# Kernel tuning notes

Measured on AMD Instinct MI355X. Metric: run time of the kernel, lower is better.

The kernel has to match this reference:

```python
import jax, jax.numpy as jnp
import numpy as np

# DeBut factor chain: each entry is [output_size, input_size, row, col, diag]
R_SHAPES = [[2048, 2048, 4, 4, 1],
            [2048, 2048, 8, 8, 4],
            [1024, 2048, 4, 8, 32],
            [512, 1024, 8, 16, 64]]
K = 4          # kernel_size
PAD = 0        # padding
IN_SIZE = 512 * K  # input_channel * kernel_size = 2048
NUM_PARAMS = sum(o * c for (o, _, _, c, _) in R_SHAPES)  # 40960


def setup_inputs() -> dict:
    key = jax.random.key(0)
    k1, k2, k3 = jax.random.split(key, 3)
    x = jax.random.normal(k1, (16, 512, 2048), dtype=jnp.float32)
    twiddle = jax.random.normal(k2, (NUM_PARAMS,), dtype=jnp.float32) * (1.0 / np.sqrt(2.0))
    bound = 1.0 / np.sqrt(IN_SIZE)
    bias = jax.random.uniform(k3, (512,), dtype=jnp.float32, minval=-bound, maxval=bound)
    return {"x": x, "twiddle": twiddle, "bias": bias}


def _pre_process(x):
    # x: (B, C, L) -> im2col rows (B*l_out, K*C), matching torch unfold + permute(0,3,2,1)
    B, C, L = x.shape
    l_out = L + 2 * PAD - (K - 1)
    xp = jnp.pad(x, ((0, 0), (0, 0), (PAD, PAD)))
    # (B, C, K, l_out): window offset axis (small fixed loop over K)
    win = jnp.stack([xp[:, :, i:i + l_out] for i in range(K)], axis=2)
    # -> (B, l_out, K, C) -> (B*l_out, K*C)
    return win.transpose(0, 3, 2, 1).reshape(B * l_out, K * C), l_out


def _debut_mult(rows, twiddle):
    # rows: (N, in_size); chain of block-diagonal butterfly factors
    out = rows
    p = 0
    for (osz, isz, row, col, diag) in R_SHAPES:
        g = isz // (col * diag)          # number of blocks
        n_p = col * osz
        # t: (g, row, col, diag)
        t = twiddle[p:p + n_p].reshape(g, diag, row, col).transpose(0, 2, 3, 1)
        xr = out.reshape(-1, g, col, diag)
        # contract over col within each block: (N, g, row, diag)
        out = jnp.einsum('grcd,bgcd->bgrd', t, xr)
        p += n_p
    return out.reshape(out.shape[0], -1)  # (N, out_size)


def reference(x, twiddle, bias):
    B, C, L = x.shape
    rows, l_out = _pre_process(x)
    out = _debut_mult(rows, twiddle) + bias
    # (B, l_out, out_channel) -> (B, out_channel, l_out)
    return out.reshape(B, l_out, -1).transpose(0, 2, 1)
```

## Files before the change

kernel.cpp:

```cpp
#include <hip/hip_runtime.h>

#define L_IN   2048
#define C_IN   512
#define L_OUT  2045
#define XT_PAD 21
#define CS     520
#define DS2    1218
#define AS2    38

typedef short short8 __attribute__((ext_vector_type(8)));
typedef float float4v __attribute__((ext_vector_type(4)));

__device__ __forceinline__ unsigned short bf16r(float f) {
    unsigned u = __float_as_uint(f);
    unsigned r = (u + 0x7FFFu + ((u >> 16) & 1u)) >> 16;
    return (unsigned short)r;
}

__global__ __launch_bounds__(256)
void build_wf(const float* __restrict__ tw, unsigned short* __restrict__ W21f,
              unsigned short* __restrict__ W43f) {
    int id = blockIdx.x * 256 + threadIdx.x;
    if (id < 65536) {
        int p = id & 7, lane = (id >> 3) & 63, oh = (id >> 9) & 1, g = id >> 10;
        int a = oh * 16 + (lane & 15);
        int e = ((lane >> 4) & 3) * 8 + p;
        int r2 = a >> 2, d2 = a & 3, c2 = e >> 2, c1 = e & 3;
        float v = tw[8192 + ((g * 4 + d2) * 8 + r2) * 8 + c2]
                * tw[(g * 8 + c2) * 16 + d2 * 4 + c1];
        W21f[id] = bf16r(v);
    } else if (id < 98304) {
        int id2 = id - 65536;
        int p = id2 & 7, lane = (id2 >> 3) & 63, kh = (id2 >> 9) & 1, s = id2 >> 10;
        int u = lane & 15;
        int w = kh * 32 + ((lane >> 4) & 3) * 8 + p;
        int r4 = u >> 1, hi = u & 1, d4 = hi * 32 + s, p2 = w >> 3, c3 = w & 7;
        float v = 0.f;
        #pragma unroll
        for (int lo = 0; lo < 2; ++lo)
            v += tw[32768 + (d4 * 8 + r4) * 16 + (2 * p2 + lo)]
               * tw[24576 + ((p2 * 32 + s) * 4 + (2 * lo + hi)) * 8 + c3];
        W43f[id2] = bf16r(v);
    }
}

__global__ __launch_bounds__(512)
void debut_fused_mfma(const unsigned short* __restrict__ W21f,
                      const unsigned short* __restrict__ W43f,
                      const float* __restrict__ x,
                      const float* __restrict__ bias, float* __restrict__ out) {
    __shared__ unsigned short xtile[20 * CS];
    __shared__ unsigned int   out2[9736];

    const int bid = blockIdx.x;
    const int swz = (bid & 7) * 256 + (bid >> 3);
    const int lt = swz & 127, b = swz >> 7;
    const int l0 = lt * 16;
    const int t = threadIdx.x;
    const int lane = t & 63, wv = t >> 6;
    const int lr = lane & 15, lh = lane >> 4;

    const float* xb = x + (size_t)b * C_IN * L_IN;

    {
        const int lq = t & 3;
        #pragma unroll
        for (int pass = 0; pass < 4; ++pass) {
            int cc = pass * 128 + (t >> 2);
            float4 v = *reinterpret_cast<const float4*>(xb + (size_t)cc * L_IN + l0 + lq * 4);
            int base = (lq * 4) * CS + cc;
            xtile[base         ] = bf16r(v.x);
            xtile[base + CS    ] = bf16r(v.y);
            xtile[base + 2 * CS] = bf16r(v.z);
            xtile[base + 3 * CS] = bf16r(v.w);
        }
        int cc = t;
        int lx = l0 + 16; if (lx > L_IN - 4) lx = L_IN - 4;
        float4 v = *reinterpret_cast<const float4*>(xb + (size_t)cc * L_IN + lx);
        int base = 16 * CS + cc;
        xtile[base         ] = bf16r(v.x);
        xtile[base + CS    ] = bf16r(v.y);
        xtile[base + 2 * CS] = bf16r(v.z);
        xtile[base + 3 * CS] = bf16r(v.w);
    }

    short8 wa[4][2];
    #pragma unroll
    for (int si = 0; si < 4; ++si) {
        int s = wv * 4 + si;
        wa[si][0] = *(const short8*)(W43f + ((size_t)(s * 2 + 0) * 64 + lane) * 8);
        wa[si][1] = *(const short8*)(W43f + ((size_t)(s * 2 + 1) * 64 + lane) * 8);
    }

    __syncthreads();

    float4v accB[4] = {};

    #pragma unroll
    for (int p = 0; p < 2; ++p) {
        const int koff = 2 * p + (wv >> 2);
        const unsigned short* xrow = &xtile[(lr + koff) * CS + lh * 8];

        #pragma unroll
        for (int gi = 0; gi < 4; ++gi) {
            const int gp = wv * 4 + gi;
            const int g  = p * 32 + gp;
            short8 vfrag = *(const short8*)(xrow + (gp & 15) * 32);
            #pragma unroll
            for (int oh = 0; oh < 2; ++oh) {
                short8 wfrag = *(const short8*)(W21f + ((size_t)(g * 2 + oh) * 64 + lane) * 8);
                float4v acc = {};
                acc = __builtin_amdgcn_mfma_f32_16x16x32_bf16(vfrag, wfrag, acc, 0, 0, 0);
                const int a = oh * 16 + lr;
                unsigned d0 = (unsigned)bf16r(acc[0]) | ((unsigned)bf16r(acc[1]) << 16);
                unsigned d1 = (unsigned)bf16r(acc[2]) | ((unsigned)bf16r(acc[3]) << 16);
                out2[(lh * 2 + 0) * DS2 + a * AS2 + gp] = d0;
                out2[(lh * 2 + 1) * DS2 + a * AS2 + gp] = d1;
            }
        }
        __syncthreads();

        #pragma unroll
        for (int si = 0; si < 4; ++si) {
            const int s = wv * 4 + si;
            const int rb = (lr >> 1) * DS2 + s * AS2 + lh * 8;
            uint2 q0 = *(const uint2*)&out2[rb + 0];
            uint2 q1 = *(const uint2*)&out2[rb + 2];
            uint2 q2 = *(const uint2*)&out2[rb + 4];
            uint2 q3 = *(const uint2*)&out2[rb + 6];
            unsigned w0, w1, w2, w3;
            if (lr & 1) {
                w0 = (q0.x >> 16) | (q0.y & 0xffff0000u);
                w1 = (q1.x >> 16) | (q1.y & 0xffff0000u);
                w2 = (q2.x >> 16) | (q2.y & 0xffff0000u);
                w3 = (q3.x >> 16) | (q3.y & 0xffff0000u);
            } else {
                w0 = (q0.x & 0xffffu) | (q0.y << 16);
                w1 = (q1.x & 0xffffu) | (q1.y << 16);
                w2 = (q2.x & 0xffffu) | (q2.y << 16);
                w3 = (q3.x & 0xffffu) | (q3.y << 16);
            }
            uint4 uw{w0, w1, w2, w3};
            short8 bb = *reinterpret_cast<short8*>(&uw);
            accB[si] = __builtin_amdgcn_mfma_f32_16x16x32_bf16(wa[si][p], bb, accB[si], 0, 0, 0);
        }
        if (p == 0) __syncthreads();
    }

    const int lpos = l0 + lr;
    if (lpos < L_OUT) {
        #pragma unroll
        for (int si = 0; si < 4; ++si) {
            const int s = wv * 4 + si;
            #pragma unroll
            for (int i = 0; i < 4; ++i) {
                int o4 = s + 32 * (lh * 4 + i);
                out[((size_t)(b * 512 + o4)) * L_OUT + lpos] = accB[si][i] + bias[o4];
            }
        }
    }
}

__global__ __launch_bounds__(256)
void debut_fused_kernel(const float* __restrict__ x,
                        const float* __restrict__ tw,
                        const float* __restrict__ bias,
                        float* __restrict__ out)
{
    __shared__ float xt[C_IN * XT_PAD];
    __shared__ float bufA[2048];
    __shared__ float bufB[2048];
    const int tile = blockIdx.x, b = blockIdx.y;
    const int l0 = tile * 16;
    const int tid = threadIdx.x;
    const float* xb = x + (size_t)b * C_IN * L_IN;
    for (int idx = tid; idx < C_IN * 19; idx += 256) {
        int c = idx / 19, ll = idx - c * 19, l = l0 + ll;
        xt[c * XT_PAD + ll] = (l < L_IN) ? xb[c * L_IN + l] : 0.0f;
    }
    __syncthreads();
    const float* t1 = tw; const float* t2 = tw + 8192;
    const float* t3 = tw + 24576; const float* t4 = tw + 32768;
    for (int rr = 0; rr < 16; ++rr) {
        const int l = l0 + rr;
        if (l >= L_OUT) break;
        #pragma unroll
        for (int i = 0; i < 8; ++i) {
            int o = tid + 256 * i, gb = o >> 2, k = gb >> 7, cb = (gb & 127) << 2;
            const float4 tq = *reinterpret_cast<const float4*>(t1 + o * 4);
            const float* xp = &xt[cb * XT_PAD + rr + k];
            bufA[o] = tq.x * xp[0] + tq.y * xp[XT_PAD] + tq.z * xp[2 * XT_PAD] + tq.w * xp[3 * XT_PAD];
        }
        __syncthreads();
        #pragma unroll
        for (int i = 0; i < 8; ++i) {
            int o = tid + 256 * i, gb = o >> 5, r = (o >> 2) & 7, d = o & 3;
            const float* tp = t2 + (((gb << 2) + d) * 8 + r) * 8;
            const float* ip = &bufA[(gb << 5) + d];
            float acc = 0.0f;
            #pragma unroll
            for (int c = 0; c < 8; ++c) acc += tp[c] * ip[c << 2];
            bufB[o] = acc;
        }
        __syncthreads();
        #pragma unroll
        for (int i = 0; i < 4; ++i) {
            int o = tid + 256 * i, gb = o >> 7, r = (o >> 5) & 3, d = o & 31;
            const float* tp = t3 + (((gb << 5) + d) * 4 + r) * 8;
            const float* ip = &bufB[(gb << 8) + d];
            float acc = 0.0f;
            #pragma unroll
            for (int c = 0; c < 8; ++c) acc += tp[c] * ip[c << 5];
            bufA[o] = acc;
        }
        __syncthreads();
        #pragma unroll
        for (int i = 0; i < 2; ++i) {
            int o = tid + 256 * i, r = o >> 6, d = o & 63;
            const float* tp = t4 + ((d << 3) + r) * 16;
            float acc = 0.0f;
            #pragma unroll
            for (int c = 0; c < 16; ++c) acc += tp[c] * bufA[(c << 6) + d];
            out[((size_t)(b * 512 + o)) * L_OUT + l] = acc + bias[o];
        }
        __syncthreads();
    }
}

extern "C" void kernel_launch(void* const* d_in, const int* in_sizes, int n_in,
                              void* d_out, int out_size, void* d_ws, size_t ws_size,
                              hipStream_t stream) {
    const float* x    = (const float*)d_in[0];
    const float* tw   = (const float*)d_in[1];
    const float* bias = (const float*)d_in[2];
    float* out = (float*)d_out;

    const size_t W21_B = 65536 * 2;
    const size_t W43_B = 32768 * 2;

    if (ws_size < W21_B + W43_B) {
        dim3 grid(128, 16);
        debut_fused_kernel<<<grid, dim3(256), 0, stream>>>(x, tw, bias, out);
        return;
    }

    unsigned short* W21f = (unsigned short*)d_ws;
    unsigned short* W43f = (unsigned short*)((char*)d_ws + W21_B);

    build_wf<<<dim3(384), dim3(256), 0, stream>>>(tw, W21f, W43f);
    debut_fused_mfma<<<dim3(2048), dim3(512), 0, stream>>>(W21f, W43f, x, bias, out);
}
```

Baseline: 46.26 us.

## Process two L-tiles per block and prefetch the next x tile during compute

Each block now handles two consecutive 16-wide L tiles, halving the grid to 1024 blocks. It loads the second tile's x data into registers while computing the first tile, then writes it to shared memory after storing the first tile's output. The aim is to hide global load latency and amortise the W43 fragment loads and block setup over two tiles. The cost is higher register pressure from the prefetch buffer and fewer blocks for occupancy and tail balance.

```diff
diff --git a/kernel.cpp b/kernel.cpp
--- a/kernel.cpp
+++ b/kernel.cpp
@@ -45,44 +45,22 @@
 }
 
 __global__ __launch_bounds__(512)
-void debut_fused_mfma(const unsigned short* __restrict__ W21f,
-                      const unsigned short* __restrict__ W43f,
-                      const float* __restrict__ x,
-                      const float* __restrict__ bias, float* __restrict__ out) {
+void debut_fused2(const unsigned short* __restrict__ W21f,
+                  const unsigned short* __restrict__ W43f,
+                  const float* __restrict__ x,
+                  const float* __restrict__ bias, float* __restrict__ out) {
     __shared__ unsigned short xtile[20 * CS];
     __shared__ unsigned int   out2[9736];
 
     const int bid = blockIdx.x;
-    const int swz = (bid & 7) * 256 + (bid >> 3);
-    const int lt = swz & 127, b = swz >> 7;
-    const int l0 = lt * 16;
+    const int swz = (bid & 7) * 128 + (bid >> 3);
+    const int ltp = swz & 63, b = swz >> 6;
     const int t = threadIdx.x;
     const int lane = t & 63, wv = t >> 6;
     const int lr = lane & 15, lh = lane >> 4;
+    const int lq = t & 3, ccq = t >> 2;
 
     const float* xb = x + (size_t)b * C_IN * L_IN;
-
-    {
-        const int lq = t & 3;
-        #pragma unroll
-        for (int pass = 0; pass < 4; ++pass) {
-            int cc = pass * 128 + (t >> 2);
-            float4 v = *reinterpret_cast<const float4*>(xb + (size_t)cc * L_IN + l0 + lq * 4);
-            int base = (lq * 4) * CS + cc;
-            xtile[base         ] = bf16r(v.x);
-            xtile[base + CS    ] = bf16r(v.y);
-            xtile[base + 2 * CS] = bf16r(v.z);
-            xtile[base + 3 * CS] = bf16r(v.w);
-        }
-        int cc = t;
-        int lx = l0 + 16; if (lx > L_IN - 4) lx = L_IN - 4;
-        float4 v = *reinterpret_cast<const float4*>(xb + (size_t)cc * L_IN + lx);
-        int base = 16 * CS + cc;
-        xtile[base         ] = bf16r(v.x);
-        xtile[base + CS    ] = bf16r(v.y);
-        xtile[base + 2 * CS] = bf16r(v.z);
-        xtile[base + 3 * CS] = bf16r(v.w);
-    }
 
     short8 wa[4][2];
     #pragma unroll
@@ -92,73 +70,140 @@
         wa[si][1] = *(const short8*)(W43f + ((size_t)(s * 2 + 1) * 64 + lane) * 8);
     }
 
+#define XLOAD(dst, L0)                                                                   \
+    do {                                                                                 \
+        _Pragma("unroll")                                                                \
+        for (int pass = 0; pass < 4; ++pass)                                             \
+            dst[pass] = *(const float4*)(xb + (size_t)(pass * 128 + ccq) * L_IN + (L0) + lq * 4); \
+        int lx = (L0) + 16; if (lx > L_IN - 4) lx = L_IN - 4;                            \
+        dst[4] = *(const float4*)(xb + (size_t)t * L_IN + lx);                           \
+    } while (0)
+
+#define XWRITE(src)                                                                      \
+    do {                                                                                 \
+        _Pragma("unroll")                                                                \
+        for (int pass = 0; pass < 4; ++pass) {                                           \
+            int base = (lq * 4) * CS + (pass * 128 + ccq);                               \
+            xtile[base         ] = bf16r(src[pass].x);                                   \
+            xtile[base + CS    ] = bf16r(src[pass].y);                                   \
+            xtile[base + 2 * CS] = bf16r(src[pass].z);                                   \
+            xtile[base + 3 * CS] = bf16r(src[pass].w);                                   \
+        }                                                                                \
+        int base = 16 * CS + t;                                                          \
+        xtile[base         ] = bf16r(src[4].x);                                          \
+        xtile[base + CS    ] = bf16r(src[4].y);                                          \
+        xtile[base + 2 * CS] = bf16r(src[4].z);                                          \
+        xtile[base + 3 * CS] = bf16r(src[4].w);                                          \
+    } while (0)
+
+#define STAGE_A(P)                                                                       \
+    do {                                                                                 \
+        const int koff = 2 * (P) + (wv >> 2);                                            \
+        const unsigned short* xrow = &xtile[(lr + koff) * CS + lh * 8];                  \
+        _Pragma("unroll")                                                                \
+        for (int gi = 0; gi < 4; ++gi) {                                                 \
+            const int gp = wv * 4 + gi;                                                  \
+            const int g  = (P) * 32 + gp;                                                \
+            short8 vfrag = *(const short8*)(xrow + (gp & 15) * 32);                      \
+            _Pragma("unroll")                                                            \
+            for (int oh = 0; oh < 2; ++oh) {                                             \
+                short8 wfrag = *(const short8*)(W21f + ((size_t)(g * 2 + oh) * 64 + lane) * 8); \
+                float4v acc = {};                                                        \
+                acc = __builtin_amdgcn_mfma_f32_16x16x32_bf16(vfrag, wfrag, acc, 0, 0, 0); \
+                const int a = oh * 16 + lr;                                              \
+                unsigned d0 = (unsigned)bf16r(acc[0]) | ((unsigned)bf16r(acc[1]) << 16); \
+                unsigned d1 = (unsigned)bf16r(acc[2]) | ((unsigned)bf16r(acc[3]) << 16); \
+                out2[(lh * 2 + 0) * DS2 + a * AS2 + gp] = d0;                            \
+                out2[(lh * 2 + 1) * DS2 + a * AS2 + gp] = d1;                            \
+            }                                                                            \
+        }                                                                                \
+    } while (0)
+
+#define STAGE_B(P, accB)                                                                 \
+    do {                                                                                 \
+        _Pragma("unroll")                                                                \
+        for (int si = 0; si < 4; ++si) {                                                 \
+            const int s = wv * 4 + si;                                                   \
+            const int rb = (lr >> 1) * DS2 + s * AS2 + lh * 8;                           \
+            uint2 q0 = *(const uint2*)&out2[rb + 0];                                     \
+            uint2 q1 = *(const uint2*)&out2[rb + 2];                                     \
+            uint2 q2 = *(const uint2*)&out2[rb + 4];                                     \
+            uint2 q3 = *(const uint2*)&out2[rb + 6];                                     \
+            unsigned w0, w1, w2, w3;                                                     \
+            if (lr & 1) {                                                                \
+                w0 = (q0.x >> 16) | (q0.y & 0xffff0000u);                                \
+                w1 = (q1.x >> 16) | (q1.y & 0xffff0000u);                                \
+                w2 = (q2.x >> 16) | (q2.y & 0xffff0000u);                                \
+                w3 = (q3.x >> 16) | (q3.y & 0xffff0000u);                                \
+            } else {                                                                     \
+                w0 = (q0.x & 0xffffu) | (q0.y << 16);                                    \
+                w1 = (q1.x & 0xffffu) | (q1.y << 16);                                    \
+                w2 = (q2.x & 0xffffu) | (q2.y << 16);                                    \
+                w3 = (q3.x & 0xffffu) | (q3.y << 16);                                    \
+            }                                                                            \
+            uint4 uw{w0, w1, w2, w3};                                                    \
+            short8 bb = *reinterpret_cast<short8*>(&uw);                                 \
+            accB[si] = __builtin_amdgcn_mfma_f32_16x16x32_bf16(wa[si][P], bb, accB[si], 0, 0, 0); \
+        }                                                                                \
+    } while (0)
+
+#define STORE(L0, accB)                                                                  \
+    do {                                                                                 \
+        const int lpos = (L0) + lr;                                                      \
+        if (lpos < L_OUT) {                                                              \
+            _Pragma("unroll")                                                            \
+            for (int si = 0; si < 4; ++si) {                                             \
+                const int s = wv * 4 + si;                                               \
+                _Pragma("unroll")                                                        \
+                for (int i = 0; i < 4; ++i) {                                            \
+                    int o4 = s + 32 * (lh * 4 + i);                                      \
+                    out[((size_t)(b * 512 + o4)) * L_OUT + lpos] = accB[si][i] + bias[o4]; \
+                }                                                                        \
+            }                                                                            \
+        }                                                                                \
+    } while (0)
+
+    const int l0a = ltp * 32;
+    const int l0b = l0a + 16;
+
+    float4 xv[5];
+    XLOAD(xv, l0a);
+    XWRITE(xv);
     __syncthreads();
 
-    float4v accB[4] = {};
-
-    #pragma unroll
-    for (int p = 0; p < 2; ++p) {
-        const int koff = 2 * p + (wv >> 2);
-        const unsigned short* xrow = &xtile[(lr + koff) * CS + lh * 8];
-
-        #pragma unroll
-        for (int gi = 0; gi < 4; ++gi) {
-            const int gp = wv * 4 + gi;
-            const int g  = p * 32 + gp;
-            short8 vfrag = *(const short8*)(xrow + (gp & 15) * 32);
-            #pragma unroll
-            for (int oh = 0; oh < 2; ++oh) {
-                short8 wfrag = *(const short8*)(W21f + ((size_t)(g * 2 + oh) * 64 + lane) * 8);
-                float4v acc = {};
-                acc = __builtin_amdgcn_mfma_f32_16x16x32_bf16(vfrag, wfrag, acc, 0, 0, 0);
-                const int a = oh * 16 + lr;
-                unsigned d0 = (unsigned)bf16r(acc[0]) | ((unsigned)bf16r(acc[1]) << 16);
-                unsigned d1 = (unsigned)bf16r(acc[2]) | ((unsigned)bf16r(acc[3]) << 16);
-                out2[(lh * 2 + 0) * DS2 + a * AS2 + gp] = d0;
-                out2[(lh * 2 + 1) * DS2 + a * AS2 + gp] = d1;
-            }
-        }
-        __syncthreads();
-
-        #pragma unroll
-        for (int si = 0; si < 4; ++si) {
-            const int s = wv * 4 + si;
-            const int rb = (lr >> 1) * DS2 + s * AS2 + lh * 8;
-            uint2 q0 = *(const uint2*)&out2[rb + 0];
-            uint2 q1 = *(const uint2*)&out2[rb + 2];
-            uint2 q2 = *(const uint2*)&out2[rb + 4];
-            uint2 q3 = *(const uint2*)&out2[rb + 6];
-            unsigned w0, w1, w2, w3;
-            if (lr & 1) {
-                w0 = (q0.x >> 16) | (q0.y & 0xffff0000u);
-                w1 = (q1.x >> 16) | (q1.y & 0xffff0000u);
-                w2 = (q2.x >> 16) | (q2.y & 0xffff0000u);
-                w3 = (q3.x >> 16) | (q3.y & 0xffff0000u);
-            } else {
-                w0 = (q0.x & 0xffffu) | (q0.y << 16);
-                w1 = (q1.x & 0xffffu) | (q1.y << 16);
-                w2 = (q2.x & 0xffffu) | (q2.y << 16);
-                w3 = (q3.x & 0xffffu) | (q3.y << 16);
-            }
-            uint4 uw{w0, w1, w2, w3};
-            short8 bb = *reinterpret_cast<short8*>(&uw);
-            accB[si] = __builtin_amdgcn_mfma_f32_16x16x32_bf16(wa[si][p], bb, accB[si], 0, 0, 0);
-        }
-        if (p == 0) __syncthreads();
-    }
-
-    const int lpos = l0 + lr;
-    if (lpos < L_OUT) {
-        #pragma unroll
-        for (int si = 0; si < 4; ++si) {
-            const int s = wv * 4 + si;
-            #pragma unroll
-            for (int i = 0; i < 4; ++i) {
-                int o4 = s + 32 * (lh * 4 + i);
-                out[((size_t)(b * 512 + o4)) * L_OUT + lpos] = accB[si][i] + bias[o4];
-            }
-        }
-    }
+    {
+        float4v accB[4] = {};
+        STAGE_A(0);
+        __syncthreads();
+        STAGE_B(0, accB);
+        float4 yv[5];
+        XLOAD(yv, l0b);
+        __syncthreads();
+        STAGE_A(1);
+        __syncthreads();
+        STAGE_B(1, accB);
+        STORE(l0a, accB);
+        XWRITE(yv);
+        __syncthreads();
+    }
+
+    {
+        float4v accB[4] = {};
+        STAGE_A(0);
+        __syncthreads();
+        STAGE_B(0, accB);
+        __syncthreads();
+        STAGE_A(1);
+        __syncthreads();
+        STAGE_B(1, accB);
+        STORE(l0b, accB);
+    }
+
+#undef XLOAD
+#undef XWRITE
+#undef STAGE_A
+#undef STAGE_B
+#undef STORE
 }
 
 __global__ __launch_bounds__(256)
@@ -248,5 +293,5 @@
     unsigned short* W43f = (unsigned short*)((char*)d_ws + W21_B);
 
     build_wf<<<dim3(384), dim3(256), 0, stream>>>(tw, W21f, W43f);
-    debut_fused_mfma<<<dim3(2048), dim3(512), 0, stream>>>(W21f, W43f, x, bias, out);
-}
+    debut_fused2<<<dim3(1024), dim3(512), 0, stream>>>(W21f, W43f, x, bias, out);
+}
```

New measurement: 63.02 us. 36.2% more time.
